# Optimization experiments

Measured on AMD Instinct MI355X. Metric: run time of the kernel, lower is better.

Reference implementation:

```python
import jax, jax.numpy as jnp
import numpy as np

EMB_DIM = 4096
OUT_DIM = 4096
T_PREV = 8192


def setup_inputs() -> dict:
    key = jax.random.key(0)
    ks = jax.random.split(key, 6)
    return {
        "x": jax.random.normal(ks[0], (1, EMB_DIM), dtype=jnp.float32),
        "W_query": jax.random.normal(ks[1], (OUT_DIM, EMB_DIM), dtype=jnp.float32) * 0.02,
        "W_key": jax.random.normal(ks[2], (OUT_DIM, EMB_DIM), dtype=jnp.float32) * 0.02,
        "W_value": jax.random.normal(ks[3], (OUT_DIM, EMB_DIM), dtype=jnp.float32) * 0.02,
        "K_cache": jax.random.normal(ks[4], (OUT_DIM, T_PREV), dtype=jnp.float32),
        "V_cache": jax.random.normal(ks[5], (OUT_DIM, T_PREV), dtype=jnp.float32),
    }


def reference(x, W_query, W_key, W_value, K_cache, V_cache):
    # x: [1, E] -> xt: [E, 1]
    xt = x.T
    q = W_query @ xt  # [D, 1]
    k = W_key @ xt    # [D, 1]
    v = W_value @ xt  # [D, 1]
    # append current step to caches (hstack semantics)
    K = jnp.concatenate([K_cache, k], axis=1)  # [D, T+1]
    V = jnp.concatenate([V_cache, v], axis=1)  # [D, T+1]
    # sigmoid-scored attention (NOT softmax)
    a = (q.reshape(1, -1) @ K) / jnp.sqrt(jnp.float32(OUT_DIM))  # [1, T+1]
    a = jax.nn.sigmoid(a)
    z = V @ a.reshape(-1, 1)  # [D, 1]
    return z
```

## Files before the change

kernel.cpp:

```cpp
#include <hip/hip_runtime.h>
#include <math.h>

#define EMB   4096
#define DIM   4096
#define TPREV 8192
#define TTOT  8193


__global__ __launch_bounds__(256) void qkv_kernel(
    const float* __restrict__ x,
    const float* __restrict__ Wq, const float* __restrict__ Wk,
    const float* __restrict__ Wv, float* __restrict__ ws) {
    float* scores = ws + 3 * DIM;
    int gtid = blockIdx.x * 256 + threadIdx.x;
    if (gtid < TTOT) scores[gtid] = 0.0f;

    int wave = threadIdx.x >> 6;
    int lane = threadIdx.x & 63;
    int g = blockIdx.x * 4 + wave;
    int m = g >> 12;
    int r = g & 4095;
    const float* W = (m == 0) ? Wq : (m == 1) ? Wk : Wv;

    const float4* row = (const float4*)(W + (size_t)r * EMB);
    const float4* xv  = (const float4*)x;

    float acc = 0.0f;
#pragma unroll
    for (int i = 0; i < EMB / 256; ++i) {
        float4 a = row[i * 64 + lane];
        float4 b = xv[i * 64 + lane];
        acc += a.x * b.x + a.y * b.y + a.z * b.z + a.w * b.w;
    }
#pragma unroll
    for (int off = 32; off > 0; off >>= 1) acc += __shfl_down(acc, off, 64);
    if (lane == 0) ws[m * DIM + r] = acc;
}

__global__ __launch_bounds__(256) void score_kernel(
    const float* __restrict__ Kc, float* __restrict__ ws) {
    const float* q    = ws;
    const float* kvec = ws + DIM;
    float* scores     = ws + 3 * DIM;

    __shared__ float qs[64];
    int d0 = blockIdx.y * 64;
    if (threadIdx.x < 64) qs[threadIdx.x] = q[d0 + threadIdx.x];
    __syncthreads();

    int t = blockIdx.x * 1024 + threadIdx.x * 4;
    if (t + 3 < TPREV) {
        float4 acc = {0.f, 0.f, 0.f, 0.f};
#pragma unroll 8
        for (int i = 0; i < 64; ++i) {
            const float4 kv = *(const float4*)(Kc + (size_t)(d0 + i) * TPREV + t);
            float qd = qs[i];
            acc.x += qd * kv.x;
            acc.y += qd * kv.y;
            acc.z += qd * kv.z;
            acc.w += qd * kv.w;
        }
        atomicAdd(&scores[t + 0], acc.x);
        atomicAdd(&scores[t + 1], acc.y);
        atomicAdd(&scores[t + 2], acc.z);
        atomicAdd(&scores[t + 3], acc.w);
    } else if (t == TPREV) {
        float s = 0.0f;
#pragma unroll 8
        for (int i = 0; i < 64; ++i) s += qs[i] * kvec[d0 + i];
        atomicAdd(&scores[TPREV], s);
    }
}

__global__ void sigmoid_kernel(float* __restrict__ ws) {
    float* scores = ws + 3 * DIM;
    int i = blockIdx.x * 256 + threadIdx.x;
    if (i < TTOT) {
        float s = scores[i] * 0.015625f;
        scores[i] = 1.0f / (1.0f + __expf(-s));
    }
}

__global__ __launch_bounds__(256) void out_kernel(
    const float* __restrict__ Vc, const float* __restrict__ ws,
    float* __restrict__ out) {
    const float* vvec = ws + 2 * DIM;
    const float* a    = ws + 3 * DIM;

    int wave = threadIdx.x >> 6;
    int lane = threadIdx.x & 63;
    int d = blockIdx.x * 4 + wave;

    const float4* row = (const float4*)(Vc + (size_t)d * TPREV);
    const float4* av  = (const float4*)a;

    float acc = 0.0f;
#pragma unroll 4
    for (int i = 0; i < TPREV / 256; ++i) {
        float4 vv = row[i * 64 + lane];
        float4 aa = av[i * 64 + lane];
        acc += vv.x * aa.x + vv.y * aa.y + vv.z * aa.z + vv.w * aa.w;
    }
#pragma unroll
    for (int off = 32; off > 0; off >>= 1) acc += __shfl_down(acc, off, 64);
    if (lane == 0) out[d] = acc + vvec[d] * a[TPREV];
}

extern "C" void kernel_launch(void* const* d_in, const int* in_sizes, int n_in,
                              void* d_out, int out_size, void* d_ws, size_t ws_size,
                              hipStream_t stream) {
    const float* x  = (const float*)d_in[0];
    const float* Wq = (const float*)d_in[1];
    const float* Wk = (const float*)d_in[2];
    const float* Wv = (const float*)d_in[3];
    const float* Kc = (const float*)d_in[4];
    const float* Vc = (const float*)d_in[5];
    float* out = (float*)d_out;
    float* ws  = (float*)d_ws;

    qkv_kernel<<<3072, 256, 0, stream>>>(x, Wq, Wk, Wv, ws);
    score_kernel<<<dim3(9, 64), 256, 0, stream>>>(Kc, ws);
    sigmoid_kernel<<<33, 256, 0, stream>>>(ws);
    out_kernel<<<1024, 256, 0, stream>>>(Vc, ws, out);
}
```

Measured before the change: 395.5 us.

## Replace atomic score accumulation with partial buffers and fused reduce-sigmoid

The score kernel now writes per-chunk partial dot products into a workspace buffer instead of issuing float atomics, using 128 chunks of 32 rows. A new reduce+sigmoid kernel sums the partials, applies the scaled sigmoid, and computes the new-token score q·k with a block reduction. This removes atomic contention and the zero-init pass, but adds about 4 MB of partial-buffer write and read traffic. Unroll factors in the qkv and output kernels are also adjusted.

```diff
diff --git a/kernel.cpp b/kernel.cpp
--- a/kernel.cpp
+++ b/kernel.cpp
@@ -6,15 +6,18 @@
 #define TPREV 8192
 #define TTOT  8193
 
+#define WS_Q        0
+#define WS_K        DIM
+#define WS_V        (2*DIM)
+#define WS_A        (3*DIM)
+#define WS_PART     20544
+#define NCHUNK      128
+#define CHUNK_ROWS  32
 
 __global__ __launch_bounds__(256) void qkv_kernel(
     const float* __restrict__ x,
     const float* __restrict__ Wq, const float* __restrict__ Wk,
     const float* __restrict__ Wv, float* __restrict__ ws) {
-    float* scores = ws + 3 * DIM;
-    int gtid = blockIdx.x * 256 + threadIdx.x;
-    if (gtid < TTOT) scores[gtid] = 0.0f;
-
     int wave = threadIdx.x >> 6;
     int lane = threadIdx.x & 63;
     int g = blockIdx.x * 4 + wave;
@@ -26,7 +29,7 @@
     const float4* xv  = (const float4*)x;
 
     float acc = 0.0f;
-#pragma unroll
+#pragma unroll 8
     for (int i = 0; i < EMB / 256; ++i) {
         float4 a = row[i * 64 + lane];
         float4 b = xv[i * 64 + lane];
@@ -39,53 +42,66 @@
 
 __global__ __launch_bounds__(256) void score_kernel(
     const float* __restrict__ Kc, float* __restrict__ ws) {
-    const float* q    = ws;
-    const float* kvec = ws + DIM;
-    float* scores     = ws + 3 * DIM;
+    const float* q = ws + WS_Q;
+    float* part    = ws + WS_PART;
 
-    __shared__ float qs[64];
-    int d0 = blockIdx.y * 64;
-    if (threadIdx.x < 64) qs[threadIdx.x] = q[d0 + threadIdx.x];
+    __shared__ float qs[CHUNK_ROWS];
+    int d0 = blockIdx.y * CHUNK_ROWS;
+    if (threadIdx.x < CHUNK_ROWS) qs[threadIdx.x] = q[d0 + threadIdx.x];
     __syncthreads();
 
     int t = blockIdx.x * 1024 + threadIdx.x * 4;
-    if (t + 3 < TPREV) {
-        float4 acc = {0.f, 0.f, 0.f, 0.f};
+    float4 acc = {0.f, 0.f, 0.f, 0.f};
 #pragma unroll 8
-        for (int i = 0; i < 64; ++i) {
-            const float4 kv = *(const float4*)(Kc + (size_t)(d0 + i) * TPREV + t);
-            float qd = qs[i];
-            acc.x += qd * kv.x;
-            acc.y += qd * kv.y;
-            acc.z += qd * kv.z;
-            acc.w += qd * kv.w;
-        }
-        atomicAdd(&scores[t + 0], acc.x);
-        atomicAdd(&scores[t + 1], acc.y);
-        atomicAdd(&scores[t + 2], acc.z);
-        atomicAdd(&scores[t + 3], acc.w);
-    } else if (t == TPREV) {
-        float s = 0.0f;
-#pragma unroll 8
-        for (int i = 0; i < 64; ++i) s += qs[i] * kvec[d0 + i];
-        atomicAdd(&scores[TPREV], s);
+    for (int i = 0; i < CHUNK_ROWS; ++i) {
+        const float4 kv = *(const float4*)(Kc + (size_t)(d0 + i) * TPREV + t);
+        float qd = qs[i];
+        acc.x += qd * kv.x;
+        acc.y += qd * kv.y;
+        acc.z += qd * kv.z;
+        acc.w += qd * kv.w;
     }
+    *(float4*)(part + (size_t)blockIdx.y * TPREV + t) = acc;
 }
 
-__global__ void sigmoid_kernel(float* __restrict__ ws) {
-    float* scores = ws + 3 * DIM;
-    int i = blockIdx.x * 256 + threadIdx.x;
-    if (i < TTOT) {
-        float s = scores[i] * 0.015625f;
-        scores[i] = 1.0f / (1.0f + __expf(-s));
+__global__ __launch_bounds__(256) void reduce_sigmoid_kernel(
+    float* __restrict__ ws) {
+    float* scores      = ws + WS_A;
+    const float* part  = ws + WS_PART;
+
+    if (blockIdx.x < 32) {
+        int t = blockIdx.x * 256 + threadIdx.x;
+        float s = 0.0f;
+#pragma unroll 16
+        for (int c = 0; c < NCHUNK; ++c) s += part[(size_t)c * TPREV + t];
+        s *= 0.015625f;
+        scores[t] = 1.0f / (1.0f + __expf(-s));
+    } else {
+        const float* q = ws + WS_Q;
+        const float* k = ws + WS_K;
+        float s = 0.0f;
+        int base = threadIdx.x * 16;
+#pragma unroll 16
+        for (int i = 0; i < 16; ++i) s += q[base + i] * k[base + i];
+        __shared__ float red[256];
+        red[threadIdx.x] = s;
+        __syncthreads();
+        for (int off = 128; off > 0; off >>= 1) {
+            if (threadIdx.x < off) red[threadIdx.x] += red[threadIdx.x + off];
+            __syncthreads();
+        }
+        if (threadIdx.x == 0) {
+            float v = red[0] * 0.015625f;
+            scores[TPREV] = 1.0f / (1.0f + __expf(-v));
+        }
     }
 }
 
 __global__ __launch_bounds__(256) void out_kernel(
     const float* __restrict__ Vc, const float* __restrict__ ws,
     float* __restrict__ out) {
-    const float* vvec = ws + 2 * DIM;
-    const float* a    = ws + 3 * DIM;
+    const float* vvec = ws + WS_V;
+    const float* a    = ws + WS_A;
 
     int wave = threadIdx.x >> 6;
     int lane = threadIdx.x & 63;
@@ -95,7 +111,7 @@
     const float4* av  = (const float4*)a;
 
     float acc = 0.0f;
-#pragma unroll 4
+#pragma unroll 8
     for (int i = 0; i < TPREV / 256; ++i) {
         float4 vv = row[i * 64 + lane];
         float4 aa = av[i * 64 + lane];
@@ -119,7 +135,7 @@
     float* ws  = (float*)d_ws;
 
     qkv_kernel<<<3072, 256, 0, stream>>>(x, Wq, Wk, Wv, ws);
-    score_kernel<<<dim3(9, 64), 256, 0, stream>>>(Kc, ws);
-    sigmoid_kernel<<<33, 256, 0, stream>>>(ws);
+    score_kernel<<<dim3(8, 128), 256, 0, stream>>>(Kc, ws);
+    reduce_sigmoid_kernel<<<33, 256, 0, stream>>>(ws);
     out_kernel<<<1024, 256, 0, stream>>>(Vc, ws, out);
 }
```

Result: no change. 399.5 us (+1.0%).
